# Kernel optimization log

Hardware: AMD Instinct MI355X
Metric: run time of the kernel (lower is better)

The kernel has to match this reference:

```python
import jax, jax.numpy as jnp
import numpy as np

B, D, H, E, K = 4096, 2048, 2048, 8, 2

def setup_inputs() -> dict:
    key = jax.random.key(0)
    k1, k2, k3 = jax.random.split(key, 3)
    x = jax.random.normal(k1, (B, D), dtype=jnp.float32)
    # keras RandomNormal(stddev=0.001) init for gating and expert kernels, zero bias
    Wg = jax.random.normal(k2, (D, E), dtype=jnp.float32) * 0.001
    bg = jnp.zeros((E,), dtype=jnp.float32)
    We = jax.random.normal(k3, (E, D, H), dtype=jnp.float32) * 0.001
    be = jnp.zeros((E, H), dtype=jnp.float32)
    return {"x": x, "Wg": Wg, "bg": bg, "We": We, "be": be}

def reference(x, Wg, bg, We, be):
    # softmax gating: [B, E]
    gating = jax.nn.softmax(x @ Wg + bg, axis=-1)
    # top-k expert selection
    topk_w, topk_idx = jax.lax.top_k(gating, K)        # [B, K]
    # dense expert stack (module runs all experts): [B, E, H]
    expert_out = jnp.einsum('bd,edh->beh', x, We) + be[None, :, :]
    # gather_nd equivalent: pick top-k experts per token -> [B, K, H]
    topk_out = jnp.take_along_axis(expert_out, topk_idx[:, :, None], axis=1)
    # weighted combine: [B, H]
    combined = jnp.sum(topk_out * topk_w[:, :, None], axis=1)
    return combined
```

## Files before the change

kernel.cpp:

```cpp
#include <hip/hip_runtime.h>
#include <hip/hip_bf16.h>
#include <stdint.h>
#include <stddef.h>

#define B_TOK 4096
#define D_DIM 2048
#define H_DIM 2048
#define E_NUM 8
#define MAX_SLOTS 72

typedef __bf16 bf16;
typedef __attribute__((ext_vector_type(8))) __bf16 bf16x8;
typedef __attribute__((ext_vector_type(4))) __bf16 bf16x4;
typedef __attribute__((ext_vector_type(4))) float f32x4;

#define WS_COUNTS   0
#define WS_ENTRIES  4096
#define WS_TKIDX    135168
#define WS_TKW      167936
#define WS_XBF      262144
#define WS_WET      17039360
#define WS_AUX      84148224ULL
#define WS_BIG_NEED 84148224ULL
#define WS_SPLIT_NEED 117702656ULL

__device__ __forceinline__ void gload16(const void* g, void* l) {
  __builtin_amdgcn_global_load_lds(
      (const __attribute__((address_space(1))) void*)g,
      (__attribute__((address_space(3))) void*)l, 16, 0, 0);
}

__global__ void zero_counts(int* counts) {
  counts[threadIdx.x] = 0;
}

__global__ __launch_bounds__(256) void gating_dot(
    const float* __restrict__ x,
    const float* __restrict__ Wg,
    const float* __restrict__ bg,
    int* __restrict__ tk_idx, float* __restrict__ tk_w,
    bf16* __restrict__ xbf) {
  __shared__ __align__(16) float part[64][68];
  __shared__ float tot[64];
  int tid = threadIdx.x;
  int b0 = blockIdx.x * 8;

  f32x4 wg[16];
  {
    const float* wgp = Wg + (size_t)tid * 64;
#pragma unroll
    for (int i = 0; i < 16; i++) wg[i] = *(const f32x4*)(wgp + 4 * i);
  }

  float acc[8][8];
#pragma unroll
  for (int tk = 0; tk < 8; tk++)
#pragma unroll
    for (int e = 0; e < 8; e++) acc[tk][e] = 0.f;

#pragma unroll
  for (int tk = 0; tk < 8; tk++) {
    const float* xr = x + (size_t)(b0 + tk) * D_DIM + tid * 8;
    f32x4 xa = *(const f32x4*)xr;
    f32x4 xc = *(const f32x4*)(xr + 4);
    if (xbf) {
      bf16x4 ba, bb;
#pragma unroll
      for (int j = 0; j < 4; j++) { ba[j] = (bf16)xa[j]; bb[j] = (bf16)xc[j]; }
      bf16* xo = xbf + (size_t)(b0 + tk) * D_DIM + tid * 8;
      *(bf16x4*)xo = ba;
      *(bf16x4*)(xo + 4) = bb;
    }
#pragma unroll
    for (int j = 0; j < 4; j++) {
#pragma unroll
      for (int e = 0; e < 4; e++) {
        acc[tk][e]     += xa[j] * wg[2 * j][e];
        acc[tk][e + 4] += xa[j] * wg[2 * j + 1][e];
        acc[tk][e]     += xc[j] * wg[2 * j + 8][e];
        acc[tk][e + 4] += xc[j] * wg[2 * j + 9][e];
      }
    }
  }

  int lane = tid & 63, w = tid >> 6;
#pragma unroll
  for (int tk = 0; tk < 8; tk++)
#pragma unroll
    for (int e = 0; e < 8; e++) {
      float v = acc[tk][e];
      v += __shfl_xor(v, 1, 64);
      v += __shfl_xor(v, 2, 64);
      if ((lane & 3) == 0)
        part[tk * 8 + e][w * 16 + (lane >> 2)] = v;
    }
  __syncthreads();

  {
    int p = tid >> 2, q = tid & 3;
    f32x4 s4 = (f32x4){0.f, 0.f, 0.f, 0.f};
#pragma unroll
    for (int i = 0; i < 4; i++) {
      f32x4 v = *(const f32x4*)&part[p][q * 16 + 4 * i];
#pragma unroll
      for (int j = 0; j < 4; j++) s4[j] += v[j];
    }
    float s = (s4[0] + s4[1]) + (s4[2] + s4[3]);
    s += __shfl_xor(s, 1, 64);
    s += __shfl_xor(s, 2, 64);
    if (q == 0) tot[p] = s;
  }
  __syncthreads();

  if (tid < 8) {
    int b = b0 + tid;
    float lg[E_NUM];
#pragma unroll
    for (int e = 0; e < E_NUM; e++) lg[e] = tot[tid * 8 + e] + bg[e];
    int i0 = 0; float v0 = lg[0];
#pragma unroll
    for (int e = 1; e < E_NUM; e++) if (lg[e] > v0) { v0 = lg[e]; i0 = e; }
    int i1 = -1; float v1 = -1e30f;
#pragma unroll
    for (int e = 0; e < E_NUM; e++)
      if (e != i0 && lg[e] > v1) { v1 = lg[e]; i1 = e; }
    float m = v0;
    float den = 0.f, p0 = 0.f, p1 = 0.f;
#pragma unroll
    for (int e = 0; e < E_NUM; e++) {
      float pe = expf(lg[e] - m);
      den += pe;
      if (e == i0) p0 = pe;
      if (e == i1) p1 = pe;
    }
    tk_idx[2 * b] = i0;
    tk_idx[2 * b + 1] = i1;
    tk_w[2 * b] = p0 / den;
    tk_w[2 * b + 1] = p1 / den;
  }
}

__global__ __launch_bounds__(256) void prefill_kernel(
    const float* __restrict__ be,
    const int* __restrict__ tk_idx,
    const float* __restrict__ tk_w,
    float* __restrict__ out) {
  int idx = blockIdx.x * blockDim.x + threadIdx.x;
  int b = idx >> 9;
  int hc = (idx & 511) * 4;
  int e0 = tk_idx[2 * b], e1 = tk_idx[2 * b + 1];
  float w0 = tk_w[2 * b], w1 = tk_w[2 * b + 1];
  f32x4 b0 = *(const f32x4*)(be + (size_t)e0 * H_DIM + hc);
  f32x4 b1 = *(const f32x4*)(be + (size_t)e1 * H_DIM + hc);
  f32x4 o;
#pragma unroll
  for (int j = 0; j < 4; j++) o[j] = w0 * b0[j] + w1 * b1[j];
  *(f32x4*)(out + (size_t)b * H_DIM + hc) = o;
}

__global__ __launch_bounds__(256) void bucketize_kernel(
    const int* __restrict__ tk_idx, int* counts, int* entries) {
  __shared__ int cursor_s;
  __shared__ int base_s;
  int e = blockIdx.x >> 3, chunk = blockIdx.x & 7;
  int tid = threadIdx.x;
  if (tid == 0) cursor_s = 0;
  __syncthreads();

  int flat[4]; bool m[4]; int nm = 0;
#pragma unroll
  for (int j = 0; j < 4; j++) {
    flat[j] = chunk * 1024 + j * 256 + tid;
    int ee = tk_idx[flat[j]];
    m[j] = (ee == e);
    nm += m[j] ? 1 : 0;
  }
  int my_off = atomicAdd(&cursor_s, nm);
  __syncthreads();
  if (tid == 0) base_s = atomicAdd(&counts[e * 16], cursor_s);
  __syncthreads();
  int p = base_s + my_off;
#pragma unroll
  for (int j = 0; j < 4; j++)
    if (m[j]) entries[e * B_TOK + p++] = flat[j];
}

__global__ void transpose_cvt_we(const float* __restrict__ We, bf16* __restrict__ WeT) {
  __shared__ __align__(16) float tile[64][65];
  int e = blockIdx.z;
  int h0 = blockIdx.x * 64, d0 = blockIdx.y * 64;
  int t = threadIdx.x;
  int dr = t >> 2, hc = (t & 3) * 16;
  const float* src = We + ((size_t)e * D_DIM + d0 + dr) * H_DIM + h0 + hc;
#pragma unroll
  for (int i = 0; i < 4; i++)
    *(f32x4*)(&tile[dr][hc + 4 * i]) = *(const f32x4*)(src + 4 * i);
  __syncthreads();
  int lane = t & 63, w = t >> 6;
#pragma unroll
  for (int s = 0; s < 2; s++) {
    int c = w * 2 + s;
    int n16 = c & 3, kslab = c >> 2;
    int nl = n16 * 16 + (lane & 15);
    int kl = kslab * 32 + (lane >> 4) * 8;
    bf16x8 v;
#pragma unroll
    for (int j = 0; j < 8; j++) v[j] = (bf16)tile[kl + j][nl];
    int gh = h0 + nl, gd = d0 + kl;
    int ntile = gh >> 7, n = gh & 127;
    int k0 = gd >> 5;
    size_t slab = ((size_t)((e * 16 + ntile) * 64 + k0)) * 4096;
    int off = ((n >> 4) * 512) + lane * 8;
    *(bf16x8*)(WeT + slab + off) = v;
  }
}

__global__ __launch_bounds__(256) void moe_gemm_fast(
    const bf16* __restrict__ xbf, const bf16* __restrict__ WeT,
    const int* __restrict__ counts, const int* __restrict__ entries,
    const float* __restrict__ tk_w, float* __restrict__ out,
    float* __restrict__ aux) {
  __shared__ __align__(16) bf16 As_s[3 * 4096];
  __shared__ __align__(16) bf16 Bs_s[3 * 4096];
  int bid = blockIdx.x;
  int slot = bid >> 4, ntile = bid & 15;
  int e = -1, toff = 0, cnt = 0;
  {
    int tot = 0;
#pragma unroll
    for (int i = 0; i < E_NUM; i++) {
      int c = counts[i * 16];
      int t = (c + 127) >> 7;
      if (slot >= tot && slot < tot + t) { e = i; toff = tot; cnt = c; }
      tot += t;
    }
  }
  if (e < 0) return;
  int mtile = slot - toff;
  int n0 = ntile * 128;
  int tid = threadIdx.x, lane = tid & 63, w = tid >> 6;
  int r = lane & 15, q = lane >> 4;
  const int* ereg = entries + e * B_TOK;
  const bf16* wet_nt = WeT + ((size_t)(e * 16 + ntile) * 64) * 4096;

  const bf16* srcA[2];
  const bf16* srcB[2];
  int chunk_off[2];
#pragma unroll
  for (int j = 0; j < 2; j++) {
    int ci = w * 2 + j;
    int m = mtile * 128 + 16 * ci + r;
    int tok = ereg[min(m, cnt - 1)] >> 1;
    srcA[j] = xbf + (size_t)tok * D_DIM + 8 * q;
    chunk_off[j] = ci * 512;
    srcB[j] = wet_nt + chunk_off[j] + lane * 8;
  }
  int wm4 = (w & 1) * 4, wn4 = (w >> 1) * 4;

  f32x4 acc[4][4];
#pragma unroll
  for (int i = 0; i < 4; i++)
#pragma unroll
    for (int j = 0; j < 4; j++) acc[i][j] = (f32x4){0.f, 0.f, 0.f, 0.f};

#pragma unroll
  for (int p = 0; p < 2; p++) {
#pragma unroll
    for (int j = 0; j < 2; j++) {
      gload16(srcA[j] + p * 32, As_s + p * 4096 + chunk_off[j]);
      gload16(srcB[j] + p * 4096, Bs_s + p * 4096 + chunk_off[j]);
    }
  }

  int pc = 0, pb = 2;
  for (int it = 0; it < 63; it++) {
    asm volatile("s_waitcnt vmcnt(4)\n\ts_barrier" ::: "memory");
    if (it < 62) {
      int kk = (it + 2) * 32;
#pragma unroll
      for (int j = 0; j < 2; j++) {
        gload16(srcA[j] + kk, As_s + pb * 4096 + chunk_off[j]);
        gload16(srcB[j] + (size_t)(it + 2) * 4096, Bs_s + pb * 4096 + chunk_off[j]);
      }
    }
    {
      const bf16* Ab = As_s + pc * 4096;
      const bf16* Bb = Bs_s + pc * 4096;
      bf16x8 af[4], bfr[4];
#pragma unroll
      for (int i = 0; i < 4; i++)
        af[i] = *(const bf16x8*)(Ab + (wm4 + i) * 512 + lane * 8);
#pragma unroll
      for (int j = 0; j < 4; j++)
        bfr[j] = *(const bf16x8*)(Bb + (wn4 + j) * 512 + lane * 8);
#pragma unroll
      for (int i = 0; i < 4; i++)
#pragma unroll
        for (int j = 0; j < 4; j++)
          acc[i][j] = __builtin_amdgcn_mfma_f32_16x16x32_bf16(af[i], bfr[j],
                                                              acc[i][j], 0, 0, 0);
    }
    pc = (pc == 2) ? 0 : pc + 1;
    pb = (pb == 2) ? 0 : pb + 1;
  }
  asm volatile("s_waitcnt vmcnt(0)\n\ts_barrier" ::: "memory");
  {
    const bf16* Ab = As_s + pc * 4096;
    const bf16* Bb = Bs_s + pc * 4096;
    bf16x8 af[4], bfr[4];
#pragma unroll
    for (int i = 0; i < 4; i++)
      af[i] = *(const bf16x8*)(Ab + (wm4 + i) * 512 + lane * 8);
#pragma unroll
    for (int j = 0; j < 4; j++)
      bfr[j] = *(const bf16x8*)(Bb + (wn4 + j) * 512 + lane * 8);
#pragma unroll
    for (int i = 0; i < 4; i++)
#pragma unroll
      for (int j = 0; j < 4; j++)
        acc[i][j] = __builtin_amdgcn_mfma_f32_16x16x32_bf16(af[i], bfr[j],
                                                            acc[i][j], 0, 0, 0);
  }

  int base_r = mtile * 128, wm = (w & 1) * 64, wn = (w >> 1) * 64;
#pragma unroll
  for (int i = 0; i < 4; i++)
#pragma unroll
    for (int reg = 0; reg < 4; reg++) {
      int rg = base_r + wm + 16 * i + q * 4 + reg;
      if (rg < cnt) {
        int ent = ereg[rg];
        int tok = ent >> 1, slotk = ent & 1;
        float wgt = tk_w[2 * tok + slotk];
        if (aux) {
          float* dst = (slotk ? aux : out) + (size_t)tok * H_DIM + n0 + wn;
#pragma unroll
          for (int j = 0; j < 4; j++)
            dst[16 * j + r] = wgt * acc[i][j][reg];
        } else {
          float* orow = out + (size_t)tok * H_DIM + n0 + wn;
#pragma unroll
          for (int j = 0; j < 4; j++)
            atomicAdd(orow + 16 * j + r, wgt * acc[i][j][reg]);
        }
      }
    }
}

__global__ __launch_bounds__(256) void combine_kernel(
    const float* __restrict__ aux,
    const float* __restrict__ be,
    const int* __restrict__ tk_idx,
    const float* __restrict__ tk_w,
    float* __restrict__ out) {
  int w = threadIdx.x >> 6, lane = threadIdx.x & 63;
  int b = blockIdx.x * 4 + w;
  int e0 = tk_idx[2 * b], e1 = tk_idx[2 * b + 1];
  float w0 = tk_w[2 * b], w1 = tk_w[2 * b + 1];
  const float* be0 = be + (size_t)e0 * H_DIM;
  const float* be1 = be + (size_t)e1 * H_DIM;
  const float* arow = aux + (size_t)b * H_DIM;
  float* orow = out + (size_t)b * H_DIM;
#pragma unroll
  for (int c = 0; c < 8; c++) {
    int h = c * 256 + lane * 4;
    f32x4 o = *(const f32x4*)(orow + h);
    f32x4 a = *(const f32x4*)(arow + h);
    f32x4 v0 = *(const f32x4*)(be0 + h);
    f32x4 v1 = *(const f32x4*)(be1 + h);
#pragma unroll
    for (int j = 0; j < 4; j++) o[j] = o[j] + a[j] + w0 * v0[j] + w1 * v1[j];
    *(f32x4*)(orow + h) = o;
  }
}

__global__ __launch_bounds__(256) void moe_gemm_slow(
    const float* __restrict__ x, const float* __restrict__ We,
    const int* __restrict__ counts, const int* __restrict__ entries,
    const float* __restrict__ tk_w, float* __restrict__ out) {
  __shared__ __align__(16) bf16 As_f[4096];
  __shared__ __align__(16) bf16 Bs_f[4096];
  __shared__ __align__(16) float Braw[4096];
  int e = blockIdx.y >> 5, mtile = blockIdx.y & 31;
  int cnt = counts[e * 16];
  if (mtile * 128 >= cnt) return;
  int n0 = blockIdx.x * 128;
  int tid = threadIdx.x, lane = tid & 63, w = tid >> 6;
  int r = lane & 15, q = lane >> 4;
  const int* ereg = entries + e * B_TOK;

  const float* srcA[2]; bf16* dstA[2];
#pragma unroll
  for (int s = 0; s < 2; s++) {
    int c = tid + s * 256;
    int ci = c >> 6, qq = (c >> 4) & 3, rr = c & 15;
    int m = mtile * 128 + 16 * ci + rr;
    int tok = ereg[min(m, cnt - 1)] >> 1;
    srcA[s] = x + (size_t)tok * D_DIM + 8 * qq;
    dstA[s] = As_f + c * 8;
  }
  const float* srcBr[4]; float* dstBr[4];
#pragma unroll
  for (int i = 0; i < 4; i++) {
    int row = (w * 4 + i) * 2 + (lane >> 5);
    srcBr[i] = We + ((size_t)e * D_DIM + row) * H_DIM + n0 + (lane & 31) * 4;
    dstBr[i] = Braw + (w * 4 + i) * 256;
  }
  int n2[2], q2[2]; bf16* dstB2[2];
#pragma unroll
  for (int s = 0; s < 2; s++) {
    int c = tid + s * 256;
    n2[s] = 16 * (c >> 6) + (c & 15);
    q2[s] = (c >> 4) & 3;
    dstB2[s] = Bs_f + c * 8;
  }
  int wm4 = (w & 1) * 4, wn4 = (w >> 1) * 4;

  f32x4 acc[4][4];
#pragma unroll
  for (int i = 0; i < 4; i++)
#pragma unroll
    for (int j = 0; j < 4; j++) acc[i][j] = (f32x4){0.f, 0.f, 0.f, 0.f};

  for (int k0 = 0; k0 < D_DIM; k0 += 32) {
    __syncthreads();
#pragma unroll
    for (int i = 0; i < 4; i++)
      gload16(srcBr[i] + (size_t)k0 * H_DIM, dstBr[i]);
#pragma unroll
    for (int s = 0; s < 2; s++) {
      f32x4 a0 = *(const f32x4*)(srcA[s] + k0);
      f32x4 a1 = *(const f32x4*)(srcA[s] + k0 + 4);
      bf16x8 av;
#pragma unroll
      for (int j = 0; j < 4; j++) { av[j] = (bf16)a0[j]; av[4 + j] = (bf16)a1[j]; }
      *(bf16x8*)dstA[s] = av;
    }
    __syncthreads();
#pragma unroll
    for (int s = 0; s < 2; s++) {
      bf16x8 bv;
#pragma unroll
      for (int t2 = 0; t2 < 8; t2++)
        bv[t2] = (bf16)Braw[(8 * q2[s] + t2) * 128 + n2[s]];
      *(bf16x8*)dstB2[s] = bv;
    }
    __syncthreads();
    bf16x8 af[4], bfr[4];
#pragma unroll
    for (int i = 0; i < 4; i++)
      af[i] = *(const bf16x8*)(As_f + (wm4 + i) * 512 + lane * 8);
#pragma unroll
    for (int j = 0; j < 4; j++)
      bfr[j] = *(const bf16x8*)(Bs_f + (wn4 + j) * 512 + lane * 8);
#pragma unroll
    for (int i = 0; i < 4; i++)
#pragma unroll
      for (int j = 0; j < 4; j++)
        acc[i][j] = __builtin_amdgcn_mfma_f32_16x16x32_bf16(af[i], bfr[j],
                                                            acc[i][j], 0, 0, 0);
  }

  int base_r = mtile * 128, wm = (w & 1) * 64, wn = (w >> 1) * 64;
#pragma unroll
  for (int i = 0; i < 4; i++)
#pragma unroll
    for (int reg = 0; reg < 4; reg++) {
      int rg = base_r + wm + 16 * i + q * 4 + reg;
      if (rg < cnt) {
        int ent = ereg[rg];
        int tok = ent >> 1, slotk = ent & 1;
        float wgt = tk_w[2 * tok + slotk];
        float* orow = out + (size_t)tok * H_DIM + n0 + wn;
#pragma unroll
        for (int j = 0; j < 4; j++)
          atomicAdd(orow + 16 * j + r, wgt * acc[i][j][reg]);
      }
    }
}

extern "C" void kernel_launch(void* const* d_in, const int* in_sizes, int n_in,
                              void* d_out, int out_size, void* d_ws, size_t ws_size,
                              hipStream_t stream) {
  const float* x  = (const float*)d_in[0];
  const float* Wg = (const float*)d_in[1];
  const float* bg = (const float*)d_in[2];
  const float* We = (const float*)d_in[3];
  const float* be = (const float*)d_in[4];
  float* out = (float*)d_out;

  char* ws = (char*)d_ws;
  int*   counts   = (int*)(ws + WS_COUNTS);
  int*   entries  = (int*)(ws + WS_ENTRIES);
  int*   tk_idx   = (int*)(ws + WS_TKIDX);
  float* tk_w     = (float*)(ws + WS_TKW);
  bf16*  xbf      = (bf16*)(ws + WS_XBF);
  bf16*  WeT      = (bf16*)(ws + WS_WET);
  float* aux      = (float*)(ws + WS_AUX);

  bool big   = (ws_size >= WS_BIG_NEED);
  bool split = (ws_size >= WS_SPLIT_NEED);

  hipLaunchKernelGGL(zero_counts, dim3(1), dim3(128), 0, stream, counts);
  hipLaunchKernelGGL(gating_dot, dim3(B_TOK / 8), dim3(256), 0, stream,
                     x, Wg, bg, tk_idx, tk_w, big ? xbf : (bf16*)nullptr);
  hipLaunchKernelGGL(bucketize_kernel, dim3(64), dim3(256), 0, stream,
                     tk_idx, counts, entries);
  if (big) {
    if (!split)
      hipLaunchKernelGGL(prefill_kernel, dim3(B_TOK * H_DIM / 4 / 256), dim3(256),
                         0, stream, be, tk_idx, tk_w, out);
    hipLaunchKernelGGL(transpose_cvt_we, dim3(H_DIM / 64, D_DIM / 64, E_NUM),
                       dim3(256), 0, stream, We, WeT);
    hipLaunchKernelGGL(moe_gemm_fast, dim3(MAX_SLOTS * 16), dim3(256), 0, stream,
                       xbf, WeT, counts, entries, tk_w, out,
                       split ? aux : (float*)nullptr);
    if (split)
      hipLaunchKernelGGL(combine_kernel, dim3(B_TOK / 4), dim3(256), 0, stream,
                         aux, be, tk_idx, tk_w, out);
  } else {
    hipLaunchKernelGGL(prefill_kernel, dim3(B_TOK * H_DIM / 4 / 256), dim3(256),
                       0, stream, be, tk_idx, tk_w, out);
    hipLaunchKernelGGL(moe_gemm_slow, dim3(H_DIM / 128, E_NUM * 32), dim3(256), 0,
                       stream, x, We, counts, entries, tk_w, out);
  }
}
```

Baseline: 410.7 us.

## Merge gating, count reset and weight transpose into one prep kernel; stream B fragments from global

Gating, zeroing of the counters and the We transpose/bf16 conversion now run as block ranges of a single launch, so two launches go away and the transpose can overlap the gating work. In the MoE GEMM, the B operand is no longer staged through LDS. Each wave loads its MFMA B fragments straight from the pre-swizzled WeT layout in global memory. This halves LDS use and adds a launch-bounds occupancy hint of 4 blocks. In exchange, the B loads are issued in the same iteration they are consumed and are no longer prefetched, so their latency may end up exposed.

```diff
diff --git a/kernel.cpp b/kernel.cpp
--- a/kernel.cpp
+++ b/kernel.cpp
@@ -30,20 +30,15 @@
       (__attribute__((address_space(3))) void*)l, 16, 0, 0);
 }
 
-__global__ void zero_counts(int* counts) {
-  counts[threadIdx.x] = 0;
-}
-
-__global__ __launch_bounds__(256) void gating_dot(
-    const float* __restrict__ x,
-    const float* __restrict__ Wg,
-    const float* __restrict__ bg,
-    int* __restrict__ tk_idx, float* __restrict__ tk_w,
-    bf16* __restrict__ xbf) {
-  __shared__ __align__(16) float part[64][68];
-  __shared__ float tot[64];
+
+__device__ __forceinline__ void gating_body(
+    int bid, float* smem,
+    const float* __restrict__ x, const float* __restrict__ Wg,
+    const float* __restrict__ bg, int* __restrict__ tk_idx,
+    float* __restrict__ tk_w, bf16* __restrict__ xbf) {
+  float* tot = smem + 64 * 68;
   int tid = threadIdx.x;
-  int b0 = blockIdx.x * 8;
+  int b0 = bid * 8;
 
   f32x4 wg[16];
   {
@@ -92,7 +87,7 @@
       v += __shfl_xor(v, 1, 64);
       v += __shfl_xor(v, 2, 64);
       if ((lane & 3) == 0)
-        part[tk * 8 + e][w * 16 + (lane >> 2)] = v;
+        smem[(tk * 8 + e) * 68 + w * 16 + (lane >> 2)] = v;
     }
   __syncthreads();
 
@@ -101,7 +96,7 @@
     f32x4 s4 = (f32x4){0.f, 0.f, 0.f, 0.f};
 #pragma unroll
     for (int i = 0; i < 4; i++) {
-      f32x4 v = *(const f32x4*)&part[p][q * 16 + 4 * i];
+      f32x4 v = *(const f32x4*)(smem + p * 68 + q * 16 + 4 * i);
 #pragma unroll
       for (int j = 0; j < 4; j++) s4[j] += v[j];
     }
@@ -138,6 +133,82 @@
     tk_w[2 * b] = p0 / den;
     tk_w[2 * b + 1] = p1 / den;
   }
+}
+
+__device__ __forceinline__ void transpose_body(
+    int tb, float* smem,
+    const float* __restrict__ We, bf16* __restrict__ WeT) {
+  float (*tile)[65] = (float(*)[65])smem;
+  int hb = tb & 31, db = (tb >> 5) & 31, e = tb >> 10;
+  int h0 = hb * 64, d0 = db * 64;
+  int t = threadIdx.x;
+  int dr = t >> 2, hc = (t & 3) * 16;
+  const float* src = We + ((size_t)e * D_DIM + d0 + dr) * H_DIM + h0 + hc;
+#pragma unroll
+  for (int i = 0; i < 4; i++)
+    *(f32x4*)(&tile[dr][hc + 4 * i]) = *(const f32x4*)(src + 4 * i);
+  __syncthreads();
+  int lane = t & 63, w = t >> 6;
+#pragma unroll
+  for (int s = 0; s < 2; s++) {
+    int c = w * 2 + s;
+    int n16 = c & 3, kslab = c >> 2;
+    int nl = n16 * 16 + (lane & 15);
+    int kl = kslab * 32 + (lane >> 4) * 8;
+    bf16x8 v;
+#pragma unroll
+    for (int j = 0; j < 8; j++) v[j] = (bf16)tile[kl + j][nl];
+    int gh = h0 + nl, gd = d0 + kl;
+    int ntile = gh >> 7, n = gh & 127;
+    int k0 = gd >> 5;
+    size_t slab = ((size_t)((e * 16 + ntile) * 64 + k0)) * 4096;
+    int off = ((n >> 4) * 512) + lane * 8;
+    *(bf16x8*)(WeT + slab + off) = v;
+  }
+}
+
+__global__ __launch_bounds__(256) void prep_kernel(
+    const float* __restrict__ x, const float* __restrict__ Wg,
+    const float* __restrict__ bg, int* __restrict__ tk_idx,
+    float* __restrict__ tk_w, bf16* __restrict__ xbf,
+    const float* __restrict__ We, bf16* __restrict__ WeT,
+    int* __restrict__ counts) {
+  __shared__ __align__(16) float smem[64 * 68 + 64];
+  int bid = blockIdx.x;
+  if (bid < 512) {
+    gating_body(bid, smem, x, Wg, bg, tk_idx, tk_w, xbf);
+  } else if (bid == 512) {
+    if (threadIdx.x < 128) counts[threadIdx.x] = 0;
+  } else {
+    transpose_body(bid - 513, smem, We, WeT);
+  }
+}
+
+__global__ __launch_bounds__(256) void bucketize_kernel(
+    const int* __restrict__ tk_idx, int* counts, int* entries) {
+  __shared__ int cursor_s;
+  __shared__ int base_s;
+  int e = blockIdx.x >> 3, chunk = blockIdx.x & 7;
+  int tid = threadIdx.x;
+  if (tid == 0) cursor_s = 0;
+  __syncthreads();
+
+  int flat[4]; bool m[4]; int nm = 0;
+#pragma unroll
+  for (int j = 0; j < 4; j++) {
+    flat[j] = chunk * 1024 + j * 256 + tid;
+    int ee = tk_idx[flat[j]];
+    m[j] = (ee == e);
+    nm += m[j] ? 1 : 0;
+  }
+  int my_off = atomicAdd(&cursor_s, nm);
+  __syncthreads();
+  if (tid == 0) base_s = atomicAdd(&counts[e * 16], cursor_s);
+  __syncthreads();
+  int p = base_s + my_off;
+#pragma unroll
+  for (int j = 0; j < 4; j++)
+    if (m[j]) entries[e * B_TOK + p++] = flat[j];
 }
 
 __global__ __launch_bounds__(256) void prefill_kernel(
@@ -158,70 +229,12 @@
   *(f32x4*)(out + (size_t)b * H_DIM + hc) = o;
 }
 
-__global__ __launch_bounds__(256) void bucketize_kernel(
-    const int* __restrict__ tk_idx, int* counts, int* entries) {
-  __shared__ int cursor_s;
-  __shared__ int base_s;
-  int e = blockIdx.x >> 3, chunk = blockIdx.x & 7;
-  int tid = threadIdx.x;
-  if (tid == 0) cursor_s = 0;
-  __syncthreads();
-
-  int flat[4]; bool m[4]; int nm = 0;
-#pragma unroll
-  for (int j = 0; j < 4; j++) {
-    flat[j] = chunk * 1024 + j * 256 + tid;
-    int ee = tk_idx[flat[j]];
-    m[j] = (ee == e);
-    nm += m[j] ? 1 : 0;
-  }
-  int my_off = atomicAdd(&cursor_s, nm);
-  __syncthreads();
-  if (tid == 0) base_s = atomicAdd(&counts[e * 16], cursor_s);
-  __syncthreads();
-  int p = base_s + my_off;
-#pragma unroll
-  for (int j = 0; j < 4; j++)
-    if (m[j]) entries[e * B_TOK + p++] = flat[j];
-}
-
-__global__ void transpose_cvt_we(const float* __restrict__ We, bf16* __restrict__ WeT) {
-  __shared__ __align__(16) float tile[64][65];
-  int e = blockIdx.z;
-  int h0 = blockIdx.x * 64, d0 = blockIdx.y * 64;
-  int t = threadIdx.x;
-  int dr = t >> 2, hc = (t & 3) * 16;
-  const float* src = We + ((size_t)e * D_DIM + d0 + dr) * H_DIM + h0 + hc;
-#pragma unroll
-  for (int i = 0; i < 4; i++)
-    *(f32x4*)(&tile[dr][hc + 4 * i]) = *(const f32x4*)(src + 4 * i);
-  __syncthreads();
-  int lane = t & 63, w = t >> 6;
-#pragma unroll
-  for (int s = 0; s < 2; s++) {
-    int c = w * 2 + s;
-    int n16 = c & 3, kslab = c >> 2;
-    int nl = n16 * 16 + (lane & 15);
-    int kl = kslab * 32 + (lane >> 4) * 8;
-    bf16x8 v;
-#pragma unroll
-    for (int j = 0; j < 8; j++) v[j] = (bf16)tile[kl + j][nl];
-    int gh = h0 + nl, gd = d0 + kl;
-    int ntile = gh >> 7, n = gh & 127;
-    int k0 = gd >> 5;
-    size_t slab = ((size_t)((e * 16 + ntile) * 64 + k0)) * 4096;
-    int off = ((n >> 4) * 512) + lane * 8;
-    *(bf16x8*)(WeT + slab + off) = v;
-  }
-}
-
-__global__ __launch_bounds__(256) void moe_gemm_fast(
+__global__ __launch_bounds__(256, 4) void moe_gemm_fast(
     const bf16* __restrict__ xbf, const bf16* __restrict__ WeT,
     const int* __restrict__ counts, const int* __restrict__ entries,
     const float* __restrict__ tk_w, float* __restrict__ out,
     float* __restrict__ aux) {
   __shared__ __align__(16) bf16 As_s[3 * 4096];
-  __shared__ __align__(16) bf16 Bs_s[3 * 4096];
   int bid = blockIdx.x;
   int slot = bid >> 4, ntile = bid & 15;
   int e = -1, toff = 0, cnt = 0;
@@ -244,7 +257,6 @@
   const bf16* wet_nt = WeT + ((size_t)(e * 16 + ntile) * 64) * 4096;
 
   const bf16* srcA[2];
-  const bf16* srcB[2];
   int chunk_off[2];
 #pragma unroll
   for (int j = 0; j < 2; j++) {
@@ -253,9 +265,12 @@
     int tok = ereg[min(m, cnt - 1)] >> 1;
     srcA[j] = xbf + (size_t)tok * D_DIM + 8 * q;
     chunk_off[j] = ci * 512;
-    srcB[j] = wet_nt + chunk_off[j] + lane * 8;
   }
   int wm4 = (w & 1) * 4, wn4 = (w >> 1) * 4;
+  const bf16* srcBf[4];
+#pragma unroll
+  for (int j = 0; j < 4; j++)
+    srcBf[j] = wet_nt + (wn4 + j) * 512 + lane * 8;
 
   f32x4 acc[4][4];
 #pragma unroll
@@ -264,35 +279,30 @@
     for (int j = 0; j < 4; j++) acc[i][j] = (f32x4){0.f, 0.f, 0.f, 0.f};
 
 #pragma unroll
-  for (int p = 0; p < 2; p++) {
-#pragma unroll
-    for (int j = 0; j < 2; j++) {
+  for (int p = 0; p < 2; p++)
+#pragma unroll
+    for (int j = 0; j < 2; j++)
       gload16(srcA[j] + p * 32, As_s + p * 4096 + chunk_off[j]);
-      gload16(srcB[j] + p * 4096, Bs_s + p * 4096 + chunk_off[j]);
-    }
-  }
 
   int pc = 0, pb = 2;
   for (int it = 0; it < 63; it++) {
-    asm volatile("s_waitcnt vmcnt(4)\n\ts_barrier" ::: "memory");
+    asm volatile("s_waitcnt vmcnt(2)\n\ts_barrier" ::: "memory");
+    bf16x8 bfr[4];
+#pragma unroll
+    for (int j = 0; j < 4; j++)
+      bfr[j] = *(const bf16x8*)(srcBf[j] + (size_t)it * 4096);
     if (it < 62) {
       int kk = (it + 2) * 32;
 #pragma unroll
-      for (int j = 0; j < 2; j++) {
+      for (int j = 0; j < 2; j++)
         gload16(srcA[j] + kk, As_s + pb * 4096 + chunk_off[j]);
-        gload16(srcB[j] + (size_t)(it + 2) * 4096, Bs_s + pb * 4096 + chunk_off[j]);
-      }
     }
     {
       const bf16* Ab = As_s + pc * 4096;
-      const bf16* Bb = Bs_s + pc * 4096;
-      bf16x8 af[4], bfr[4];
+      bf16x8 af[4];
 #pragma unroll
       for (int i = 0; i < 4; i++)
         af[i] = *(const bf16x8*)(Ab + (wm4 + i) * 512 + lane * 8);
-#pragma unroll
-      for (int j = 0; j < 4; j++)
-        bfr[j] = *(const bf16x8*)(Bb + (wn4 + j) * 512 + lane * 8);
 #pragma unroll
       for (int i = 0; i < 4; i++)
 #pragma unroll
@@ -306,14 +316,13 @@
   asm volatile("s_waitcnt vmcnt(0)\n\ts_barrier" ::: "memory");
   {
     const bf16* Ab = As_s + pc * 4096;
-    const bf16* Bb = Bs_s + pc * 4096;
     bf16x8 af[4], bfr[4];
+#pragma unroll
+    for (int j = 0; j < 4; j++)
+      bfr[j] = *(const bf16x8*)(srcBf[j] + (size_t)63 * 4096);
 #pragma unroll
     for (int i = 0; i < 4; i++)
       af[i] = *(const bf16x8*)(Ab + (wm4 + i) * 512 + lane * 8);
-#pragma unroll
-    for (int j = 0; j < 4; j++)
-      bfr[j] = *(const bf16x8*)(Bb + (wn4 + j) * 512 + lane * 8);
 #pragma unroll
     for (int i = 0; i < 4; i++)
 #pragma unroll
@@ -501,17 +510,16 @@
   bool big   = (ws_size >= WS_BIG_NEED);
   bool split = (ws_size >= WS_SPLIT_NEED);
 
-  hipLaunchKernelGGL(zero_counts, dim3(1), dim3(128), 0, stream, counts);
-  hipLaunchKernelGGL(gating_dot, dim3(B_TOK / 8), dim3(256), 0, stream,
-                     x, Wg, bg, tk_idx, tk_w, big ? xbf : (bf16*)nullptr);
+  int prep_blocks = big ? (513 + 8192) : 513;
+  hipLaunchKernelGGL(prep_kernel, dim3(prep_blocks), dim3(256), 0, stream,
+                     x, Wg, bg, tk_idx, tk_w, big ? xbf : (bf16*)nullptr,
+                     We, WeT, counts);
   hipLaunchKernelGGL(bucketize_kernel, dim3(64), dim3(256), 0, stream,
                      tk_idx, counts, entries);
   if (big) {
     if (!split)
       hipLaunchKernelGGL(prefill_kernel, dim3(B_TOK * H_DIM / 4 / 256), dim3(256),
                          0, stream, be, tk_idx, tk_w, out);
-    hipLaunchKernelGGL(transpose_cvt_we, dim3(H_DIM / 64, D_DIM / 64, E_NUM),
-                       dim3(256), 0, stream, We, WeT);
     hipLaunchKernelGGL(moe_gemm_fast, dim3(MAX_SLOTS * 16), dim3(256), 0, stream,
                        xbf, WeT, counts, entries, tk_w, out,
                        split ? aux : (float*)nullptr);
```

Result: faster. 384.6 us (-6.4%).
